# Performance work log

Measured on AMD Instinct MI355X. Metric: run time of the kernel, lower is better.

## Reference

```python
import jax, jax.numpy as jnp
import numpy as np

BATCH, SEQ, INPUT_DIM, HIDDEN = 128, 1024, 256, 512


def setup_inputs() -> dict:
    key = jax.random.key(0)
    k1, k2, k3 = jax.random.split(key, 3)
    scale_su = 1.0 / np.sqrt(HIDDEN + INPUT_DIM)
    scale_out = 1.0 / np.sqrt(HIDDEN)
    return {
        "x": jax.random.normal(k1, (BATCH, SEQ, INPUT_DIM), dtype=jnp.float32),
        "carry": jnp.zeros((BATCH, HIDDEN), dtype=jnp.float32),
        "W_su": jax.random.normal(k2, (HIDDEN + INPUT_DIM, HIDDEN), dtype=jnp.float32) * scale_su,
        "b_su": jnp.zeros((HIDDEN,), dtype=jnp.float32),
        "W_out": jax.random.normal(k3, (HIDDEN, 1), dtype=jnp.float32) * scale_out,
        "b_out": jnp.zeros((1,), dtype=jnp.float32),
    }


def reference(x, carry, W_su, b_su, W_out, b_out):
    # Split state_update kernel into z-part and x-part (equivalent to concat -> Dense).
    hidden = carry.shape[-1]
    W_z = W_su[:hidden]          # (H, H)
    W_x = W_su[hidden:]          # (D, H)

    # Precompute the input contribution for all timesteps in one big GEMM.
    xW = jnp.einsum('btd,dh->bth', x, W_x) + b_su  # (B, T, H)

    def step(z, xw_t):
        z_new = jnp.tanh(z @ W_z + xw_t)
        return z_new, None

    # scan over time (T leading): (T, B, H)
    z_last, _ = jax.lax.scan(step, carry, jnp.swapaxes(xW, 0, 1))
    out = z_last @ W_out + b_out  # (B, 1)
    return out, z_last
```

## Files before the change

kernel.cpp:

```cpp
#include <hip/hip_runtime.h>
#include <hip/hip_bf16.h>

typedef _Float16 f16;
typedef _Float16 f16x2 __attribute__((ext_vector_type(2)));
typedef _Float16 f16x4 __attribute__((ext_vector_type(4)));
typedef _Float16 f16x8 __attribute__((ext_vector_type(8)));
typedef float f32x4 __attribute__((ext_vector_type(4)));

#define BATCH 128
#define SEQ   1024
#define IND   256
#define HID   512

#if defined(__has_builtin)
#if __has_builtin(__builtin_amdgcn_fdot2)
#define HAVE_FDOT2 1
#endif
#endif

__device__ __forceinline__ float fdot2(f16x2 a, f16x2 b, float c) {
#ifdef HAVE_FDOT2
  return __builtin_amdgcn_fdot2(a, b, c, false);
#else
  return c + (float)a[0] * (float)b[0] + (float)a[1] * (float)b[1];
#endif
}

union v8u {
  f16x8 v;
  f16x2 h[4];
};

__device__ __forceinline__ float tanh_fast(float s) {
  float e = __expf(2.0f * s);
  return 1.0f - 2.0f / (e + 1.0f);
}

template <int CTRL>
__device__ __forceinline__ float fdpp(float x) {
  int i = __builtin_bit_cast(int, x);
  i = __builtin_amdgcn_mov_dpp(i, CTRL, 0xf, 0xf, false);
  return __builtin_bit_cast(float, i);
}

__global__ __launch_bounds__(256) void prep_kernel(const float* __restrict__ Wsu,
                                                   f16* __restrict__ WzT,
                                                   f16* __restrict__ WxT) {
  int g = blockIdx.x * 256 + threadIdx.x;
  int k = g >> 9;
  int h = g & 511;
  float v = Wsu[g];
  if (k < HID) WzT[h * HID + k] = (f16)v;
  else         WxT[h * IND + (k - HID)] = (f16)v;
}

__global__ __launch_bounds__(256) void gemm1_kernel(const float* __restrict__ x,
                                                    const f16* __restrict__ WxT,
                                                    const float* __restrict__ bsu,
                                                    f16* __restrict__ xw) {
  const int m0 = blockIdx.x * 64, n0 = blockIdx.y * 64;
  const int w = threadIdx.x >> 6, l = threadIdx.x & 63;
  const int r16 = l & 15;
  const int kg  = l >> 4;

  const int arow = m0 + w * 16 + r16;

  f32x4 acc[4];
#pragma unroll
  for (int nt = 0; nt < 4; ++nt) {
    float bv = bsu[n0 + nt * 16 + r16];
    acc[nt] = (f32x4){bv, bv, bv, bv};
  }

#pragma unroll
  for (int kb = 0; kb < 8; ++kb) {
    const int k0 = kb * 32 + kg * 8;
    const float4* ap = (const float4*)&x[(size_t)arow * IND + k0];
    float4 a0 = ap[0], a1 = ap[1];
    f16x8 afrag = {(f16)a0.x, (f16)a0.y, (f16)a0.z, (f16)a0.w,
                   (f16)a1.x, (f16)a1.y, (f16)a1.z, (f16)a1.w};
#pragma unroll
    for (int nt = 0; nt < 4; ++nt) {
      f16x8 bfrag = *(const f16x8*)&WxT[(size_t)(n0 + nt * 16 + r16) * IND + k0];
      acc[nt] = __builtin_amdgcn_mfma_f32_16x16x32_f16(afrag, bfrag, acc[nt], 0, 0, 0);
    }
  }

#pragma unroll
  for (int nt = 0; nt < 4; ++nt) {
#pragma unroll
    for (int r = 0; r < 4; ++r) {
      int grow = m0 + w * 16 + kg * 4 + r;
      int gcol = n0 + nt * 16 + r16;
      xw[(size_t)grow * HID + gcol] = (f16)acc[nt][r];
    }
  }
}

__global__ __launch_bounds__(512, 2) void scan_kernel(
    const f16* __restrict__ WzT, const f16* __restrict__ xw,
    const float* __restrict__ carry, const float* __restrict__ Wout,
    const float* __restrict__ bout, float* __restrict__ outp) {
  __shared__ __align__(16) f16 zsh[2][512];
  __shared__ __align__(16) f16x8 wl6[8][512];
  __shared__ __align__(16) f16x8 wl7[8][512];
  __shared__ float red[512];

  const int b_ = blockIdx.x;
  const int tid = threadIdx.x;
  const int w = tid >> 6, l = tid & 63;
  const int kc = l & 7;
  const int hq = l >> 3;
  const int hbase = w * 64 + hq * 8;

  f16x2 wreg[6][32];
#pragma unroll
  for (int r = 0; r < 6; ++r) {
#pragma unroll
    for (int s = 0; s < 8; ++s) {
      v8u v;
      v.v = *(const f16x8*)&WzT[(hbase + r) * HID + kc * 64 + ((s ^ kc) & 7) * 8];
#pragma unroll
      for (int p = 0; p < 4; ++p) wreg[r][s * 4 + p] = v.h[p];
    }
  }
#pragma unroll
  for (int r = 0; r < 6; ++r) {
#pragma unroll
    for (int s = 0; s < 32; ++s) {
      unsigned u = __builtin_bit_cast(unsigned, wreg[r][s]);
      asm volatile("" : "+v"(u));
      wreg[r][s] = __builtin_bit_cast(f16x2, u);
    }
  }
#pragma unroll
  for (int s = 0; s < 8; ++s) {
    wl6[s][tid] = *(const f16x8*)&WzT[(hbase + 6) * HID + kc * 64 + ((s ^ kc) & 7) * 8];
    wl7[s][tid] = *(const f16x8*)&WzT[(hbase + 7) * HID + kc * 64 + ((s ^ kc) & 7) * 8];
  }

  zsh[0][tid] = (f16)carry[b_ * HID + tid];

  const int b0 = l & 1, b1 = (l >> 1) & 1, b2 = (l >> 2) & 1;
  const int myh = hbase + (b2 << 2) + (b0 << 1) + b1;

  float xw_cur = (float)xw[(size_t)b_ * SEQ * HID + myh];

  __syncthreads();

  float zlast = 0.f;
  for (int t = 0; t < SEQ; ++t) {
    const int p = t & 1;
    int tn = (t + 1 < SEQ) ? t + 1 : t;
    float xw_nxt = (float)xw[((size_t)b_ * SEQ + tn) * HID + myh];

    const f16* zb = &zsh[p][kc * 64];
    float a0 = 0.f, a1 = 0.f, a2 = 0.f, a3 = 0.f;
    float a4 = 0.f, a5 = 0.f, a6 = 0.f, a7 = 0.f;
#pragma unroll
    for (int s = 0; s < 8; ++s) {
      v8u zc, w6, w7;
      zc.v = *(const f16x8*)&zb[((s ^ kc) & 7) * 8];
      w6.v = wl6[s][tid];
      w7.v = wl7[s][tid];
#pragma unroll
      for (int q4 = 0; q4 < 4; ++q4) {
        f16x2 zp = zc.h[q4];
        int pi = s * 4 + q4;
        a0 = fdot2(zp, wreg[0][pi], a0);
        a1 = fdot2(zp, wreg[1][pi], a1);
        a2 = fdot2(zp, wreg[2][pi], a2);
        a3 = fdot2(zp, wreg[3][pi], a3);
        a4 = fdot2(zp, wreg[4][pi], a4);
        a5 = fdot2(zp, wreg[5][pi], a5);
        a6 = fdot2(zp, w6.h[q4], a6);
        a7 = fdot2(zp, w7.h[q4], a7);
      }
    }

    float n0_ = b2 ? a4 : a0, s0_ = b2 ? a0 : a4;
    float n1_ = b2 ? a5 : a1, s1_ = b2 ? a1 : a5;
    float n2_ = b2 ? a6 : a2, s2_ = b2 ? a2 : a6;
    float n3_ = b2 ? a7 : a3, s3_ = b2 ? a3 : a7;
    n0_ += fdpp<0x141>(s0_);
    n1_ += fdpp<0x141>(s1_);
    n2_ += fdpp<0x141>(s2_);
    n3_ += fdpp<0x141>(s3_);
    float m0_ = b0 ? n2_ : n0_, t0_ = b0 ? n0_ : n2_;
    float m1_ = b0 ? n3_ : n1_, t1_ = b0 ? n1_ : n3_;
    m0_ += fdpp<0xB1>(t0_);
    m1_ += fdpp<0xB1>(t1_);
    float f0_ = b1 ? m1_ : m0_, g0_ = b1 ? m0_ : m1_;
    float tot = f0_ + fdpp<0x4E>(g0_);

    float z = tanh_fast(tot + xw_cur);
    zlast = z;
    zsh[p ^ 1][myh] = (f16)z;
    __syncthreads();
    xw_cur = xw_nxt;
  }

  outp[BATCH + (size_t)b_ * HID + myh] = zlast;
  red[myh] = zlast * Wout[myh];
  __syncthreads();
  if (tid < 64) {
    float s2 = 0.f;
#pragma unroll
    for (int i = 0; i < 8; ++i) s2 += red[tid + 64 * i];
    red[tid] = s2;
  }
  __syncthreads();
  if (tid == 0) {
    float s3 = 0.f;
    for (int i = 0; i < 64; ++i) s3 += red[i];
    outp[b_] = s3 + bout[0];
  }
}

extern "C" void kernel_launch(void* const* d_in, const int* in_sizes, int n_in,
                              void* d_out, int out_size, void* d_ws, size_t ws_size,
                              hipStream_t stream) {
  const float* x     = (const float*)d_in[0];
  const float* carry = (const float*)d_in[1];
  const float* Wsu   = (const float*)d_in[2];
  const float* bsu   = (const float*)d_in[3];
  const float* Wout  = (const float*)d_in[4];
  const float* bout  = (const float*)d_in[5];
  float* outp = (float*)d_out;

  char* ws = (char*)d_ws;
  f16* WzT = (f16*)(ws);
  f16* WxT = (f16*)(ws + 512 * 1024);
  f16* xw  = (f16*)(ws + 768 * 1024);

  prep_kernel<<<dim3((768 * 512) / 256), 256, 0, stream>>>(Wsu, WzT, WxT);
  gemm1_kernel<<<dim3(BATCH * SEQ / 64, HID / 64), 256, 0, stream>>>(x, WxT, bsu, xw);
  scan_kernel<<<dim3(BATCH), 512, 0, stream>>>(WzT, xw, carry, Wout, bout, outp);
}
```

Before: 1.692 ms.

## Restructure input GEMM so each block computes full hidden width with LDS-staged weights

The input-projection GEMM now has each block compute all 512 output columns for its 64 rows, instead of one 64x64 tile. This means x is read and converted only once rather than eight times. Weight k-slices are double-buffered through shared memory, and the output is staged in LDS so it can be written to global memory as coalesced 16-byte stores. The cost is 128 accumulator registers per thread plus 64KB of shared memory, which could limit occupancy. The sequential scan kernel likely dominates total time, so the end-to-end effect may be small.

```diff
diff --git a/kernel.cpp b/kernel.cpp
--- a/kernel.cpp
+++ b/kernel.cpp
@@ -54,46 +54,79 @@
   else         WxT[h * IND + (k - HID)] = (f16)v;
 }
 
-__global__ __launch_bounds__(256) void gemm1_kernel(const float* __restrict__ x,
-                                                    const f16* __restrict__ WxT,
-                                                    const float* __restrict__ bsu,
-                                                    f16* __restrict__ xw) {
-  const int m0 = blockIdx.x * 64, n0 = blockIdx.y * 64;
-  const int w = threadIdx.x >> 6, l = threadIdx.x & 63;
+__global__ __launch_bounds__(256, 2) void gemm1_kernel(const float* __restrict__ x,
+                                                       const f16* __restrict__ WxT,
+                                                       const float* __restrict__ bsu,
+                                                       f16* __restrict__ xw) {
+  __shared__ __align__(16) char smem[65536];
+  f16x8* Bbuf0 = (f16x8*)smem;
+  f16x8* Bbuf1 = (f16x8*)(smem + 32768);
+
+  const int m0 = blockIdx.x * 64;
+  const int tid = threadIdx.x;
+  const int w = tid >> 6, l = tid & 63;
   const int r16 = l & 15;
   const int kg  = l >> 4;
-
   const int arow = m0 + w * 16 + r16;
 
-  f32x4 acc[4];
-#pragma unroll
-  for (int nt = 0; nt < 4; ++nt) {
-    float bv = bsu[n0 + nt * 16 + r16];
+  f32x4 acc[32];
+#pragma unroll
+  for (int nt = 0; nt < 32; ++nt) {
+    float bv = bsu[nt * 16 + r16];
     acc[nt] = (f32x4){bv, bv, bv, bv};
   }
 
 #pragma unroll
+  for (int i = 0; i < 8; ++i) {
+    int c = tid + 256 * i;
+    int n = c >> 2;
+    int g = c & 3;
+    Bbuf0[g * 512 + n] = *(const f16x8*)&WxT[(size_t)n * IND + 0 + g * 8];
+  }
+  __syncthreads();
+
+#pragma unroll
   for (int kb = 0; kb < 8; ++kb) {
-    const int k0 = kb * 32 + kg * 8;
-    const float4* ap = (const float4*)&x[(size_t)arow * IND + k0];
+    f16x8* Bc = (kb & 1) ? Bbuf1 : Bbuf0;
+    f16x8* Bn = (kb & 1) ? Bbuf0 : Bbuf1;
+    if (kb + 1 < 8) {
+      const int k0n = (kb + 1) * 32;
+#pragma unroll
+      for (int i = 0; i < 8; ++i) {
+        int c = tid + 256 * i;
+        int n = c >> 2;
+        int g = c & 3;
+        Bn[g * 512 + n] = *(const f16x8*)&WxT[(size_t)n * IND + k0n + g * 8];
+      }
+    }
+    const float4* ap = (const float4*)&x[(size_t)arow * IND + kb * 32 + kg * 8];
     float4 a0 = ap[0], a1 = ap[1];
     f16x8 afrag = {(f16)a0.x, (f16)a0.y, (f16)a0.z, (f16)a0.w,
                    (f16)a1.x, (f16)a1.y, (f16)a1.z, (f16)a1.w};
 #pragma unroll
-    for (int nt = 0; nt < 4; ++nt) {
-      f16x8 bfrag = *(const f16x8*)&WxT[(size_t)(n0 + nt * 16 + r16) * IND + k0];
+    for (int nt = 0; nt < 32; ++nt) {
+      f16x8 bfrag = Bc[kg * 512 + nt * 16 + r16];
       acc[nt] = __builtin_amdgcn_mfma_f32_16x16x32_f16(afrag, bfrag, acc[nt], 0, 0, 0);
     }
-  }
-
-#pragma unroll
-  for (int nt = 0; nt < 4; ++nt) {
+    __syncthreads();
+  }
+
+  f16* Ot = (f16*)smem;
+#pragma unroll
+  for (int nt = 0; nt < 32; ++nt) {
 #pragma unroll
     for (int r = 0; r < 4; ++r) {
-      int grow = m0 + w * 16 + kg * 4 + r;
-      int gcol = n0 + nt * 16 + r16;
-      xw[(size_t)grow * HID + gcol] = (f16)acc[nt][r];
-    }
+      int row = w * 16 + kg * 4 + r;
+      Ot[row * 512 + nt * 16 + r16] = (f16)acc[nt][r];
+    }
+  }
+  __syncthreads();
+#pragma unroll
+  for (int i = 0; i < 16; ++i) {
+    int c = tid + 256 * i;
+    int row = c >> 6;
+    int co = (c & 63) * 8;
+    *(f16x8*)&xw[(size_t)(m0 + row) * HID + co] = *(const f16x8*)&Ot[row * 512 + co];
   }
 }
 
@@ -234,6 +267,6 @@
   f16* xw  = (f16*)(ws + 768 * 1024);
 
   prep_kernel<<<dim3((768 * 512) / 256), 256, 0, stream>>>(Wsu, WzT, WxT);
-  gemm1_kernel<<<dim3(BATCH * SEQ / 64, HID / 64), 256, 0, stream>>>(x, WxT, bsu, xw);
+  gemm1_kernel<<<dim3(BATCH * SEQ / 64), 256, 0, stream>>>(x, WxT, bsu, xw);
   scan_kernel<<<dim3(BATCH), 512, 0, stream>>>(WzT, xw, carry, Wout, bout, outp);
 }
```

Result: faster. 1.441 ms, median of 2 (-14.8%).
